# Performance work log

Hardware: AMD Instinct MI355X
Metric: run time of the kernel (lower is better)

The kernel has to match this reference:

```python
import jax, jax.numpy as jnp
import numpy as np

EPS = 1e-5
K = 3

def _bn(x, g, b):
    # training-mode BatchNorm2d: batch stats over (N,H,W), biased variance
    m = jnp.mean(x, axis=(0, 2, 3), keepdims=True)
    v = jnp.var(x, axis=(0, 2, 3), keepdims=True)
    return (x - m) * jax.lax.rsqrt(v + EPS) * g[None, :, None, None] + b[None, :, None, None]

def _gelu(x):
    return jax.nn.gelu(x, approximate=False)

def _dyn_dw(x, aw1, ab1, aw2, ab2):
    # dynamic depthwise conv: per-sample k^2 softmax weights shared over channels
    b, c, h, w = x.shape
    gap = jnp.mean(x, axis=(2, 3))                              # (b,c)
    h1 = jax.nn.relu(jnp.einsum('oc,bc->bo', aw1, gap) + ab1)   # (b,c//8)
    kw = jax.nn.softmax(jnp.einsum('oc,bc->bo', aw2, h1) + ab2, axis=1)  # (b,k^2)
    xp = jnp.pad(x, ((0, 0), (0, 0), (1, 1), (1, 1)))
    out = jnp.zeros_like(x)
    idx = 0
    for i in range(K):
        for j in range(K):
            out = out + kw[:, idx, None, None, None] * xp[:, :, i:i + h, j:j + w]
            idx += 1
    return out

def _channel_att(x, w1, w2):
    avg = jnp.mean(x, axis=(2, 3))        # (b,C)
    mx = jnp.max(x, axis=(2, 3))          # (b,C)
    def fc(v):
        return jnp.einsum('oc,bc->bo', w2, jax.nn.relu(jnp.einsum('oc,bc->bo', w1, v)))
    s = jax.nn.sigmoid(fc(avg) + fc(mx))  # (b,C)
    return s[:, :, None, None] * x

def _forward(x, w1, b1, g1, be1, aw1, ab1, aw2, ab2, g2, be2,
             ca_w1, ca_w2, pw, pb, g3, be3, sw, sb):
    b, n, d = x.shape
    h = w = int(np.sqrt(n))
    residual = x
    xi = jnp.transpose(x.reshape(b, h, w, d), (0, 3, 1, 2))       # (b,d,h,w)
    # pw_expand: 1x1 conv -> GELU -> BN
    y = jnp.einsum('oc,bchw->bohw', w1, xi) + b1[None, :, None, None]
    y = _bn(_gelu(y), g1, be1)                                    # (b,4d,h,w)
    # dw_conv: dynamic depthwise -> GELU -> BN -> channel attention
    y = _dyn_dw(y, aw1, ab1, aw2, ab2)
    y = _bn(_gelu(y), g2, be2)
    y = _channel_att(y, ca_w1, ca_w2)
    # spatial attention
    avg_o = jnp.mean(y, axis=1, keepdims=True)
    max_o = jnp.max(y, axis=1, keepdims=True)
    sp_in = jnp.concatenate([avg_o, max_o], axis=1)               # (b,2,h,w)
    sp = jax.lax.conv_general_dilated(sp_in, sw, (1, 1), ((3, 3), (3, 3)),
                                      dimension_numbers=('NCHW', 'OIHW', 'NCHW'))
    sp = jax.nn.sigmoid(sp + sb[None, :, None, None])
    y = y * sp
    # pw_project: 1x1 conv -> BN
    y = jnp.einsum('oc,bchw->bohw', pw, y) + pb[None, :, None, None]
    y = _bn(y, g3, be3)
    y = jnp.transpose(y, (0, 2, 3, 1)).reshape(b, n, d)
    return residual + y

def setup_inputs() -> dict:
    key = jax.random.key(0)
    ks = jax.random.split(key, 16)
    d, C = 256, 1024
    def rn(k, shape, fan):
        return jax.random.normal(k, shape, jnp.float32) * np.float32(np.sqrt(2.0 / fan))
    return {
        'x': jax.random.normal(ks[0], (8, 1024, d), jnp.float32),
        'w1': rn(ks[1], (C, d), d), 'b1': jnp.zeros((C,), jnp.float32),
        'g1': jnp.ones((C,), jnp.float32), 'be1': jnp.zeros((C,), jnp.float32),
        'aw1': rn(ks[2], (C // 8, C), C), 'ab1': jnp.zeros((C // 8,), jnp.float32),
        'aw2': rn(ks[3], (K * K, C // 8), C // 8), 'ab2': jnp.zeros((K * K,), jnp.float32),
        'g2': jnp.ones((C,), jnp.float32), 'be2': jnp.zeros((C,), jnp.float32),
        'ca_w1': rn(ks[4], (C // 16, C), C), 'ca_w2': rn(ks[5], (C, C // 16), C // 16),
        'pw': rn(ks[6], (d, C), C), 'pb': jnp.zeros((d,), jnp.float32),
        'g3': jnp.ones((d,), jnp.float32), 'be3': jnp.zeros((d,), jnp.float32),
        'sw': rn(ks[7], (1, 2, 7, 7), 2 * 49), 'sb': jnp.zeros((1,), jnp.float32),
    }

def reference(x, w1, b1, g1, be1, aw1, ab1, aw2, ab2, g2, be2,
              ca_w1, ca_w2, pw, pb, g3, be3, sw, sb):
    return _forward(x, w1, b1, g1, be1, aw1, ab1, aw2, ab2, g2, be2,
                    ca_w1, ca_w2, pw, pb, g3, be3, sw, sb)
```

## Files before the change

### kernel.cpp

```cpp
#include <hip/hip_runtime.h>
#include <math.h>

constexpr int B = 8;
constexpr int D = 256;
constexpr int C = 1024;
constexpr int H = 32, W = 32;
constexpr int P = H * W;
constexpr int M = B * P;
constexpr float EPS = 1e-5f;

typedef unsigned short u16;
typedef unsigned int u32;
typedef __attribute__((ext_vector_type(8))) short short8;
typedef __attribute__((ext_vector_type(4))) float floatx4;

constexpr size_t WS_CHSUM1 = 0;
constexpr size_t WS_CHSQ1  = 1024;
constexpr size_t WS_GAPSUM = 2048;
constexpr size_t WS_CHSUM3 = 10240;
constexpr size_t WS_CHSQ3  = 10496;
constexpr size_t WS_ACC_COUNT = 10752;
constexpr size_t WS_SCALE1 = 11264;
constexpr size_t WS_SHIFT1 = 12288;
constexpr size_t WS_KW     = 21504;
constexpr size_t WS_SCALE2 = 21760;
constexpr size_t WS_SHIFT2 = 22784;
constexpr size_t WS_AVGBN  = 23808;
constexpr size_t WS_MXBN   = 32000;
constexpr size_t WS_SATT   = 40192;
constexpr size_t WS_AVGO   = 48384;
constexpr size_t WS_MAXO   = 56576;
constexpr size_t WS_SP     = 64768;
constexpr size_t WS_PSUM2  = 73728;
constexpr size_t WS_PSQ2   = 335872;
constexpr size_t WS_PMAX2  = 598016;
constexpr size_t WS_PMIN2  = 860160;
constexpr size_t WS_PRE    = 1122304;
constexpr size_t WS_T1B    = 3219456;
constexpr size_t WS_T2B    = 7413760;
constexpr size_t WS_XB     = 11608064;
constexpr size_t WS_W1B    = 12656640;
constexpr size_t WS_PWB    = 12787712;
constexpr size_t WS_YB     = 12918784;

__device__ __forceinline__ float gelu_exact(float v) {
    return 0.5f * v * (1.0f + erff(v * 0.70710678118654752440f));
}

__device__ __forceinline__ u16 f2bf(float f) {
    u32 u = __float_as_uint(f);
    u += 0x7fff + ((u >> 16) & 1);
    return (u16)(u >> 16);
}

__device__ __forceinline__ float bf2f(u16 v) {
    return __uint_as_float(((u32)v) << 16);
}

__global__ __launch_bounds__(256) void cvt_all_kernel(const float* __restrict__ x,
                                                      const float* __restrict__ w1,
                                                      const float* __restrict__ pw,
                                                      u16* __restrict__ xb,
                                                      u16* __restrict__ w1b,
                                                      u16* __restrict__ pwb) {
    const int i = blockIdx.x * 256 + threadIdx.x;
    const float* src;
    u16* dst;
    int off;
    if (i < 524288)      { src = x;  dst = xb;  off = i; }
    else if (i < 589824) { src = w1; dst = w1b; off = i - 524288; }
    else                 { src = pw; dst = pwb; off = i - 589824; }
    const float4 v = *(const float4*)(src + (size_t)off * 4);
    uint2 o;
    o.x = ((u32)f2bf(v.x)) | ((u32)f2bf(v.y) << 16);
    o.y = ((u32)f2bf(v.z)) | ((u32)f2bf(v.w) << 16);
    *(uint2*)(dst + (size_t)off * 4) = o;
}

template<int KD, int EPI, int NS, int MB, int NB>
__global__ __launch_bounds__(256) void mfma_gemm_kernel(
    const u16* __restrict__ A,
    const u16* __restrict__ Bw,
    const float* __restrict__ bias,
    const float* __restrict__ rowscale,
    void* __restrict__ outv,
    float* __restrict__ csum,
    float* __restrict__ csq,
    float* __restrict__ gsum)
{
    constexpr int MI = MB / 32;
    constexpr int NJ = NB / 32;
    extern __shared__ u16 smem[];
    u16* As = smem;
    u16* Bs = smem + MB * 32;
    const int t = threadIdx.x;
    const int lane = t & 63;
    const int row0 = blockIdx.y * MB;
    const int col0 = blockIdx.x * NB;
    const int wv = t >> 6;
    const int wrow = (wv >> 1) * (MB / 2);
    const int wcol = (wv & 1) * (NB / 2);
    const int lm = lane & 15;
    const int lk8 = (lane >> 4) * 8;

    const int srow = t >> 2;
    const int scol = (t & 3) * 8;

    const u16* gA0 = A + (size_t)(row0 + srow) * KD + scol;
    const u16* gA1 = A + (size_t)(row0 + 64 + srow) * KD + scol;
    const u16* gB0 = Bw + (size_t)(col0 + srow) * KD + scol;

    const floatx4 zero = {0.f, 0.f, 0.f, 0.f};
    floatx4 acc[MI][NJ];
#pragma unroll
    for (int i = 0; i < MI; ++i)
#pragma unroll
        for (int j = 0; j < NJ; ++j) acc[i][j] = zero;

    for (int k0 = 0; k0 < KD; k0 += 32) {
        __builtin_amdgcn_global_load_lds(
            (const __attribute__((address_space(1))) void*)(gA0 + k0),
            (__attribute__((address_space(3))) void*)(As + t * 8), 16, 0, 0);
        if (MB == 128)
            __builtin_amdgcn_global_load_lds(
                (const __attribute__((address_space(1))) void*)(gA1 + k0),
                (__attribute__((address_space(3))) void*)(As + 2048 + t * 8), 16, 0, 0);
        __builtin_amdgcn_global_load_lds(
            (const __attribute__((address_space(1))) void*)(gB0 + k0),
            (__attribute__((address_space(3))) void*)(Bs + t * 8), 16, 0, 0);
        __syncthreads();
        short8 af[MI], bf[NJ];
#pragma unroll
        for (int i = 0; i < MI; ++i)
            af[i] = *(const short8*)(As + (wrow + i * 16 + lm) * 32 + lk8);
#pragma unroll
        for (int j = 0; j < NJ; ++j)
            bf[j] = *(const short8*)(Bs + (wcol + j * 16 + lm) * 32 + lk8);
#pragma unroll
        for (int i = 0; i < MI; ++i)
#pragma unroll
            for (int j = 0; j < NJ; ++j)
                acc[i][j] = __builtin_amdgcn_mfma_f32_16x16x32_bf16(af[i], bf[j], acc[i][j], 0, 0, 0);
        __syncthreads();
    }

    float colsum[NJ], colsq[NJ];
#pragma unroll
    for (int j = 0; j < NJ; ++j) { colsum[j] = 0.f; colsq[j] = 0.f; }

    if (EPI == 0) {
        u16* Cs = smem;
#pragma unroll
        for (int i = 0; i < MI; ++i) {
#pragma unroll
            for (int r = 0; r < 4; ++r) {
                const int lrow = wrow + i * 16 + (lane >> 4) * 4 + r;
#pragma unroll
                for (int j = 0; j < NJ; ++j) {
                    const int lcol = wcol + j * 16 + lm;
                    const float tv = gelu_exact(acc[i][j][r] + bias[col0 + lcol]);
                    Cs[lrow * NB + lcol] = f2bf(tv);
                    colsum[j] += tv;
                    colsq[j] = fmaf(tv, tv, colsq[j]);
                }
            }
        }
        __syncthreads();
        const int rr = t >> 1;
        const int hh = (t & 1) * 32;
        u16* outp = (u16*)outv + (size_t)(row0 + rr) * NS + col0 + hh;
#pragma unroll
        for (int k = 0; k < 4; ++k) {
            *(uint4*)(outp + k * 8) = *(const uint4*)(Cs + rr * NB + hh + k * 8);
        }
    } else {
#pragma unroll
        for (int i = 0; i < MI; ++i) {
#pragma unroll
            for (int r = 0; r < 4; ++r) {
                const int grow = row0 + wrow + i * 16 + (lane >> 4) * 4 + r;
                const float rs = rowscale[grow];
#pragma unroll
                for (int j = 0; j < NJ; ++j) {
                    const int gcol = col0 + wcol + j * 16 + lm;
                    const float tv = rs * acc[i][j][r] + bias[gcol];
                    ((float*)outv)[(size_t)grow * NS + gcol] = tv;
                    colsum[j] += tv;
                    colsq[j] = fmaf(tv, tv, colsq[j]);
                }
            }
        }
    }

    const int bb = (blockIdx.y * MB) >> 10;
#pragma unroll
    for (int j = 0; j < NJ; ++j) {
        float s = colsum[j];
        float q = colsq[j];
        s += __shfl_xor(s, 16); s += __shfl_xor(s, 32);
        q += __shfl_xor(q, 16); q += __shfl_xor(q, 32);
        if (lane < 16) {
            const int c = col0 + wcol + j * 16 + lm;
            atomicAdd(&csum[c], s);
            atomicAdd(&csq[c], q);
            if (EPI == 0) atomicAdd(&gsum[bb * NS + c], s);
        }
    }
}

__global__ __launch_bounds__(1024) void dynmlp_kernel(const float* __restrict__ chsum1,
                                                      const float* __restrict__ chsq1,
                                                      const float* __restrict__ gapsum,
                                                      const float* __restrict__ g1,
                                                      const float* __restrict__ be1,
                                                      const float* __restrict__ aw1,
                                                      const float* __restrict__ ab1,
                                                      const float* __restrict__ aw2,
                                                      const float* __restrict__ ab2,
                                                      float* __restrict__ scale1,
                                                      float* __restrict__ shift1,
                                                      float* __restrict__ kw) {
    const int b = blockIdx.x;
    const int t = threadIdx.x;
    const int wave = t >> 6, lane = t & 63;
    __shared__ float g[1024];
    __shared__ float h1[128];
    __shared__ float logits[12];
    {
        const float m = chsum1[t] * (1.0f / (float)M);
        const float var = chsq1[t] * (1.0f / (float)M) - m * m;
        const float rstd = rsqrtf(var + EPS);
        const float sc = rstd * g1[t];
        const float sh = be1[t] - m * sc;
        if (b == 0) { scale1[t] = sc; shift1[t] = sh; }
        g[t] = gapsum[b * C + t] * (1.0f / (float)P) * sc + sh;
    }
    __syncthreads();
#pragma unroll
    for (int k = 0; k < 8; ++k) {
        const int u = wave * 8 + k;
        const float4* wr = (const float4*)(aw1 + (size_t)u * C);
        float s = 0.f;
#pragma unroll
        for (int ch = 0; ch < 4; ++ch) {
            const float4 wv = wr[lane + 64 * ch];
            const float4 sv = *(const float4*)(g + 4 * lane + 256 * ch);
            s += wv.x * sv.x + wv.y * sv.y + wv.z * sv.z + wv.w * sv.w;
        }
#pragma unroll
        for (int off = 1; off < 64; off <<= 1) s += __shfl_xor(s, off);
        if (lane == 0) h1[u] = fmaxf(s + ab1[u], 0.f);
    }
    __syncthreads();
    if (wave < 9) {
        float s = aw2[wave * 128 + lane] * h1[lane]
                + aw2[wave * 128 + 64 + lane] * h1[64 + lane];
#pragma unroll
        for (int off = 1; off < 64; off <<= 1) s += __shfl_xor(s, off);
        if (lane == 0) logits[wave] = s + ab2[wave];
    }
    __syncthreads();
    if (t == 0) {
        float mx = logits[0];
        for (int i = 1; i < 9; ++i) mx = fmaxf(mx, logits[i]);
        float e[9], den = 0.f;
        for (int i = 0; i < 9; ++i) { e[i] = expf(logits[i] - mx); den += e[i]; }
        const float inv = 1.0f / den;
        for (int i = 0; i < 9; ++i) kw[b * 9 + i] = e[i] * inv;
    }
}

__global__ __launch_bounds__(256) void dwconv_kernel(const u16* __restrict__ t1b,
                                                     const float* __restrict__ scale1,
                                                     const float* __restrict__ shift1,
                                                     const float* __restrict__ kw,
                                                     u16* __restrict__ t2b,
                                                     float* __restrict__ psum,
                                                     float* __restrict__ psq,
                                                     float* __restrict__ pmax,
                                                     float* __restrict__ pmin) {
    const int b = blockIdx.y >> 5;
    const int h = blockIdx.y & 31;
    const int c0 = (blockIdx.x * 256 + threadIdx.x) * 2;
    float k[9];
#pragma unroll
    for (int i = 0; i < 9; ++i) k[i] = kw[b * 9 + i];
    const float sc0 = scale1[c0],     sh0 = shift1[c0];
    const float sc1 = scale1[c0 + 1], sh1 = shift1[c0 + 1];
    const u16* base = t1b + (size_t)b * P * C + c0;
    const bool rok[3] = { h > 0, true, h < H - 1 };

    float2 win[3][3];
    const float2 z = {0.f, 0.f};
#pragma unroll
    for (int ri = 0; ri < 3; ++ri) {
        win[ri][0] = z;
#pragma unroll
        for (int ci = 1; ci < 3; ++ci) {
            if (rok[ri]) {
                const u32 v = *(const u32*)(base + ((size_t)((h + ri - 1) * W + (ci - 1))) * C);
                float2 r;
                r.x = fmaf(bf2f((u16)(v & 0xffff)), sc0, sh0);
                r.y = fmaf(bf2f((u16)(v >> 16)),    sc1, sh1);
                win[ri][ci] = r;
            } else win[ri][ci] = z;
        }
    }

    float s0 = 0.f, q0 = 0.f, mx0 = -INFINITY, mn0 = INFINITY;
    float s1 = 0.f, q1 = 0.f, mx1 = -INFINITY, mn1 = INFINITY;
    for (int w = 0; w < W; ++w) {
        float a0 = 0.f, a1 = 0.f;
#pragma unroll
        for (int ri = 0; ri < 3; ++ri)
#pragma unroll
            for (int ci = 0; ci < 3; ++ci) {
                a0 = fmaf(k[ri * 3 + ci], win[ri][ci].x, a0);
                a1 = fmaf(k[ri * 3 + ci], win[ri][ci].y, a1);
            }
        const float y0 = gelu_exact(a0);
        const float y1 = gelu_exact(a1);
        *(u32*)(t2b + ((size_t)b * P + h * W + w) * C + c0) =
            ((u32)f2bf(y0)) | ((u32)f2bf(y1) << 16);
        s0 += y0; q0 = fmaf(y0, y0, q0); mx0 = fmaxf(mx0, y0); mn0 = fminf(mn0, y0);
        s1 += y1; q1 = fmaf(y1, y1, q1); mx1 = fmaxf(mx1, y1); mn1 = fminf(mn1, y1);
        if (w < W - 1) {
#pragma unroll
            for (int ri = 0; ri < 3; ++ri) {
                win[ri][0] = win[ri][1];
                win[ri][1] = win[ri][2];
                if (rok[ri] && (w + 2 < W)) {
                    const u32 v = *(const u32*)(base + ((size_t)((h + ri - 1) * W + (w + 2))) * C);
                    float2 r;
                    r.x = fmaf(bf2f((u16)(v & 0xffff)), sc0, sh0);
                    r.y = fmaf(bf2f((u16)(v >> 16)),    sc1, sh1);
                    win[ri][2] = r;
                } else win[ri][2] = z;
            }
        }
    }
    const int idx = b * 32 + h;
    psum[c0 * 256 + idx] = s0;  psum[(c0 + 1) * 256 + idx] = s1;
    psq [c0 * 256 + idx] = q0;  psq [(c0 + 1) * 256 + idx] = q1;
    pmax[c0 * 256 + idx] = mx0; pmax[(c0 + 1) * 256 + idx] = mx1;
    pmin[c0 * 256 + idx] = mn0; pmin[(c0 + 1) * 256 + idx] = mn1;
}

__global__ __launch_bounds__(256) void stats2_kernel(const float* __restrict__ psum,
                                                     const float* __restrict__ psq,
                                                     const float* __restrict__ pmax,
                                                     const float* __restrict__ pmin,
                                                     const float* __restrict__ g2,
                                                     const float* __restrict__ be2,
                                                     float* __restrict__ scale2,
                                                     float* __restrict__ shift2,
                                                     float* __restrict__ avgbn,
                                                     float* __restrict__ mxbn) {
    const int c = blockIdx.x;
    const int t = threadIdx.x;
    const int base = c * 256 + t;
    float s  = psum[base];
    float q  = psq[base];
    float mx = pmax[base];
    float mn = pmin[base];
#pragma unroll
    for (int off = 1; off < 32; off <<= 1) {
        s += __shfl_xor(s, off);
        q += __shfl_xor(q, off);
        mx = fmaxf(mx, __shfl_xor(mx, off));
        mn = fminf(mn, __shfl_xor(mn, off));
    }
    __shared__ float bs[8], bq[8], bmx[8], bmn[8];
    __shared__ float sc_sh[2];
    if ((t & 31) == 0) {
        const int b = t >> 5;
        bs[b] = s; bq[b] = q; bmx[b] = mx; bmn[b] = mn;
    }
    __syncthreads();
    if (t == 0) {
        float S = 0.f, Q = 0.f;
#pragma unroll
        for (int b = 0; b < 8; ++b) { S += bs[b]; Q += bq[b]; }
        const float m = S * (1.0f / (float)M);
        const float var = Q * (1.0f / (float)M) - m * m;
        const float rstd = rsqrtf(var + EPS);
        const float sc = rstd * g2[c];
        const float sh = be2[c] - m * sc;
        scale2[c] = sc;
        shift2[c] = sh;
        sc_sh[0] = sc; sc_sh[1] = sh;
    }
    __syncthreads();
    if (t < 8) {
        const float sc = sc_sh[0], sh = sc_sh[1];
        avgbn[t * C + c] = bs[t] * (1.0f / (float)P) * sc + sh;
        mxbn[t * C + c] = (sc >= 0.f ? bmx[t] : bmn[t]) * sc + sh;
    }
}

__global__ __launch_bounds__(1024) void chatt_kernel(const float* __restrict__ avgbn,
                                                     const float* __restrict__ mxbn,
                                                     const float* __restrict__ caw1,
                                                     const float* __restrict__ caw2,
                                                     float* __restrict__ s_att) {
    const int b = blockIdx.x;
    const int t = threadIdx.x;
    const int wave = t >> 6, lane = t & 63;
    __shared__ float la[1024], lx[1024], ha[64], hm[64];
    la[t] = avgbn[b * C + t];
    lx[t] = mxbn[b * C + t];
    __syncthreads();
#pragma unroll
    for (int k = 0; k < 8; ++k) {
        const int u = wave * 8 + k;
        const int row = u & 63;
        const float* src = (u < 64) ? la : lx;
        const float4* wr = (const float4*)(caw1 + (size_t)row * C);
        float s = 0.f;
#pragma unroll
        for (int ch = 0; ch < 4; ++ch) {
            const float4 wv = wr[lane + 64 * ch];
            const float4 sv = *(const float4*)(src + 4 * lane + 256 * ch);
            s += wv.x * sv.x + wv.y * sv.y + wv.z * sv.z + wv.w * sv.w;
        }
#pragma unroll
        for (int off = 1; off < 64; off <<= 1) s += __shfl_xor(s, off);
        if (lane == 0) {
            s = fmaxf(s, 0.f);
            if (u < 64) ha[row] = s; else hm[row] = s;
        }
    }
    __syncthreads();
    {
        const float4* w2 = (const float4*)(caw2 + (size_t)t * 64);
        float s = 0.f;
#pragma unroll
        for (int j = 0; j < 16; ++j) {
            const float4 wv = w2[j];
            s += wv.x * (ha[j * 4 + 0] + hm[j * 4 + 0]);
            s += wv.y * (ha[j * 4 + 1] + hm[j * 4 + 1]);
            s += wv.z * (ha[j * 4 + 2] + hm[j * 4 + 2]);
            s += wv.w * (ha[j * 4 + 3] + hm[j * 4 + 3]);
        }
        s_att[b * C + t] = 1.0f / (1.0f + expf(-s));
    }
}

__global__ __launch_bounds__(256) void yq_kernel(const u16* __restrict__ t2b,
                                                 const float* __restrict__ scale2,
                                                 const float* __restrict__ shift2,
                                                 const float* __restrict__ s_att,
                                                 u16* __restrict__ yb,
                                                 float* __restrict__ avg_o,
                                                 float* __restrict__ max_o) {
    const int row = blockIdx.x;
    const int b = row >> 10;
    const int t = threadIdx.x;
    const int c0 = t * 4;
    const uint2 vv = *(const uint2*)(t2b + (size_t)row * C + c0);
    const float v0 = bf2f((u16)(vv.x & 0xffff));
    const float v1 = bf2f((u16)(vv.x >> 16));
    const float v2 = bf2f((u16)(vv.y & 0xffff));
    const float v3 = bf2f((u16)(vv.y >> 16));
    const float4 sc = *(const float4*)(scale2 + c0);
    const float4 sh = *(const float4*)(shift2 + c0);
    const float4 sa = *(const float4*)(s_att + (size_t)b * C + c0);
    const float y0 = fmaf(v0, sc.x, sh.x) * sa.x;
    const float y1 = fmaf(v1, sc.y, sh.y) * sa.y;
    const float y2 = fmaf(v2, sc.z, sh.z) * sa.z;
    const float y3 = fmaf(v3, sc.w, sh.w) * sa.w;
    uint2 o;
    o.x = ((u32)f2bf(y0)) | ((u32)f2bf(y1) << 16);
    o.y = ((u32)f2bf(y2)) | ((u32)f2bf(y3) << 16);
    *(uint2*)(yb + (size_t)row * C + c0) = o;
    float s = (y0 + y1) + (y2 + y3);
    float mx = fmaxf(fmaxf(y0, y1), fmaxf(y2, y3));
#pragma unroll
    for (int off = 32; off > 0; off >>= 1) {
        s += __shfl_down(s, off);
        mx = fmaxf(mx, __shfl_down(mx, off));
    }
    __shared__ float ss[4], sm[4];
    const int wave = t >> 6, lane = t & 63;
    if (lane == 0) { ss[wave] = s; sm[wave] = mx; }
    __syncthreads();
    if (t == 0) {
        const float S = ss[0] + ss[1] + ss[2] + ss[3];
        const float Mx = fmaxf(fmaxf(sm[0], sm[1]), fmaxf(sm[2], sm[3]));
        avg_o[row] = S * (1.0f / (float)C);
        max_o[row] = Mx;
    }
}

__global__ __launch_bounds__(1024) void spconv_kernel(const float* __restrict__ avg_o,
                                                      const float* __restrict__ max_o,
                                                      const float* __restrict__ sw,
                                                      const float* __restrict__ sb,
                                                      float* __restrict__ sp) {
    const int b = blockIdx.x;
    const int t = threadIdx.x;
    __shared__ float pa[P], pm[P], wsh[98];
    pa[t] = avg_o[b * P + t];
    pm[t] = max_o[b * P + t];
    if (t < 98) wsh[t] = sw[t];
    const float sbv = sb[0];
    __syncthreads();
    const int h = t >> 5, w = t & 31;
    float acc = sbv;
#pragma unroll
    for (int i = 0; i < 7; ++i) {
        const int hh = h + i - 3;
        if (hh < 0 || hh >= H) continue;
#pragma unroll
        for (int j = 0; j < 7; ++j) {
            const int ww = w + j - 3;
            if (ww < 0 || ww >= W) continue;
            const int pidx = hh * W + ww;
            acc = fmaf(wsh[i * 7 + j], pa[pidx], acc);
            acc = fmaf(wsh[49 + i * 7 + j], pm[pidx], acc);
        }
    }
    sp[b * P + t] = 1.0f / (1.0f + expf(-acc));
}

__global__ __launch_bounds__(256) void final_kernel(const float* __restrict__ x,
                                                    const float* __restrict__ pre,
                                                    const float* __restrict__ chsum3,
                                                    const float* __restrict__ chsq3,
                                                    const float* __restrict__ g3,
                                                    const float* __restrict__ be3,
                                                    float* __restrict__ out) {
    __shared__ float lsc[256], lsh[256];
    const int t = threadIdx.x;
    {
        const float m = chsum3[t] * (1.0f / (float)M);
        const float var = chsq3[t] * (1.0f / (float)M) - m * m;
        const float rstd = rsqrtf(var + EPS);
        const float sc = rstd * g3[t];
        lsc[t] = sc;
        lsh[t] = be3[t] - m * sc;
    }
    __syncthreads();
    const int i = blockIdx.x * 256 + t;
    const int e = i * 4;
    const int d = e & 255;
    const float4 xv = *(const float4*)(x + e);
    const float4 pv = *(const float4*)(pre + e);
    const float4 sc = *(const float4*)(lsc + d);
    const float4 sh = *(const float4*)(lsh + d);
    float4 o;
    o.x = xv.x + fmaf(pv.x, sc.x, sh.x);
    o.y = xv.y + fmaf(pv.y, sc.y, sh.y);
    o.z = xv.z + fmaf(pv.z, sc.z, sh.z);
    o.w = xv.w + fmaf(pv.w, sc.w, sh.w);
    *(float4*)(out + e) = o;
}

extern "C" void kernel_launch(void* const* d_in, const int* in_sizes, int n_in,
                              void* d_out, int out_size, void* d_ws, size_t ws_size,
                              hipStream_t stream) {
    const float* x    = (const float*)d_in[0];
    const float* w1   = (const float*)d_in[1];
    const float* b1   = (const float*)d_in[2];
    const float* g1   = (const float*)d_in[3];
    const float* be1  = (const float*)d_in[4];
    const float* aw1  = (const float*)d_in[5];
    const float* ab1  = (const float*)d_in[6];
    const float* aw2  = (const float*)d_in[7];
    const float* ab2  = (const float*)d_in[8];
    const float* g2   = (const float*)d_in[9];
    const float* be2  = (const float*)d_in[10];
    const float* caw1 = (const float*)d_in[11];
    const float* caw2 = (const float*)d_in[12];
    const float* pw   = (const float*)d_in[13];
    const float* pb   = (const float*)d_in[14];
    const float* g3   = (const float*)d_in[15];
    const float* be3  = (const float*)d_in[16];
    const float* sw   = (const float*)d_in[17];
    const float* sb   = (const float*)d_in[18];
    float* out = (float*)d_out;
    float* ws = (float*)d_ws;

    hipMemsetAsync(ws, 0, WS_ACC_COUNT * sizeof(float), stream);

    float* chsum1  = ws + WS_CHSUM1;
    float* chsq1   = ws + WS_CHSQ1;
    float* gapsum  = ws + WS_GAPSUM;
    float* chsum3  = ws + WS_CHSUM3;
    float* chsq3   = ws + WS_CHSQ3;
    float* scale1  = ws + WS_SCALE1;
    float* shift1  = ws + WS_SHIFT1;
    float* kw      = ws + WS_KW;
    float* scale2  = ws + WS_SCALE2;
    float* shift2  = ws + WS_SHIFT2;
    float* avgbn   = ws + WS_AVGBN;
    float* mxbn    = ws + WS_MXBN;
    float* s_att   = ws + WS_SATT;
    float* avg_o   = ws + WS_AVGO;
    float* max_o   = ws + WS_MAXO;
    float* sp      = ws + WS_SP;
    float* psum2   = ws + WS_PSUM2;
    float* psq2    = ws + WS_PSQ2;
    float* pmax2   = ws + WS_PMAX2;
    float* pmin2   = ws + WS_PMIN2;
    float* pre     = ws + WS_PRE;
    u16* t1b = (u16*)(ws + WS_T1B);
    u16* t2b = (u16*)(ws + WS_T2B);
    u16* xb  = (u16*)(ws + WS_XB);
    u16* w1b = (u16*)(ws + WS_W1B);
    u16* pwb = (u16*)(ws + WS_PWB);
    u16* yb  = (u16*)(ws + WS_YB);

    cvt_all_kernel<<<dim3(2560), 256, 0, stream>>>(x, w1, pw, xb, w1b, pwb);
    mfma_gemm_kernel<256, 0, C, 128, 64><<<dim3(C / 64, M / 128), 256, 16384, stream>>>(
        xb, w1b, b1, nullptr, t1b, chsum1, chsq1, gapsum);
    dynmlp_kernel<<<dim3(B), 1024, 0, stream>>>(chsum1, chsq1, gapsum, g1, be1,
                                                aw1, ab1, aw2, ab2, scale1, shift1, kw);
    dwconv_kernel<<<dim3(C / 512, B * H), 256, 0, stream>>>(t1b, scale1, shift1, kw, t2b,
                                                            psum2, psq2, pmax2, pmin2);
    stats2_kernel<<<dim3(C), 256, 0, stream>>>(psum2, psq2, pmax2, pmin2, g2, be2,
                                               scale2, shift2, avgbn, mxbn);
    chatt_kernel<<<dim3(B), 1024, 0, stream>>>(avgbn, mxbn, caw1, caw2, s_att);
    yq_kernel<<<dim3(M), 256, 0, stream>>>(t2b, scale2, shift2, s_att, yb, avg_o, max_o);
    spconv_kernel<<<dim3(B), 1024, 0, stream>>>(avg_o, max_o, sw, sb, sp);
    mfma_gemm_kernel<1024, 1, D, 64, 64><<<dim3(D / 64, M / 64), 256, 8192, stream>>>(
        yb, pwb, pb, sp, pre, chsum3, chsq3, nullptr);
    final_kernel<<<dim3((M * D / 4) / 256), 256, 0, stream>>>(x, pre, chsum3, chsq3, g3, be3, out);
}
```

Measured before the change: 218.9 us.

## Replace dwconv partial-stat buffers with atomics and fold stats2 into chatt

The depthwise conv kernel now reduces its per-row sum, sum-of-squares, max and min straight into per-channel and per-batch accumulators with atomicAdd and atomicMax on order-preserving float keys, instead of writing partial arrays. The separate stats2 kernel is removed, and the channel-attention kernel now computes BN2 scale/shift and the pooled stats itself. The memset is folded into the convert kernel, which zeroes the accumulator region. This removes two launches and a large partial-stat round trip, at the cost of atomic contention and non-deterministic summation order.

```diff
diff --git a/kernel.cpp b/kernel.cpp
--- a/kernel.cpp
+++ b/kernel.cpp
@@ -19,29 +19,28 @@
 constexpr size_t WS_GAPSUM = 2048;
 constexpr size_t WS_CHSUM3 = 10240;
 constexpr size_t WS_CHSQ3  = 10496;
-constexpr size_t WS_ACC_COUNT = 10752;
-constexpr size_t WS_SCALE1 = 11264;
-constexpr size_t WS_SHIFT1 = 12288;
-constexpr size_t WS_KW     = 21504;
-constexpr size_t WS_SCALE2 = 21760;
-constexpr size_t WS_SHIFT2 = 22784;
-constexpr size_t WS_AVGBN  = 23808;
-constexpr size_t WS_MXBN   = 32000;
-constexpr size_t WS_SATT   = 40192;
-constexpr size_t WS_AVGO   = 48384;
-constexpr size_t WS_MAXO   = 56576;
-constexpr size_t WS_SP     = 64768;
-constexpr size_t WS_PSUM2  = 73728;
-constexpr size_t WS_PSQ2   = 335872;
-constexpr size_t WS_PMAX2  = 598016;
-constexpr size_t WS_PMIN2  = 860160;
-constexpr size_t WS_PRE    = 1122304;
-constexpr size_t WS_T1B    = 3219456;
-constexpr size_t WS_T2B    = 7413760;
-constexpr size_t WS_XB     = 11608064;
-constexpr size_t WS_W1B    = 12656640;
-constexpr size_t WS_PWB    = 12787712;
-constexpr size_t WS_YB     = 12918784;
+constexpr size_t WS_CHSUM2 = 10752;
+constexpr size_t WS_CHSQ2  = 11776;
+constexpr size_t WS_BSUM2  = 12800;
+constexpr size_t WS_UMAX2  = 20992;
+constexpr size_t WS_UMAXN2 = 29184;
+constexpr size_t WS_ACC_COUNT = 37376;
+constexpr size_t WS_SCALE1 = 37376;
+constexpr size_t WS_SHIFT1 = 38400;
+constexpr size_t WS_KW     = 39424;
+constexpr size_t WS_SCALE2 = 39680;
+constexpr size_t WS_SHIFT2 = 40704;
+constexpr size_t WS_SATT   = 41728;
+constexpr size_t WS_AVGO   = 49920;
+constexpr size_t WS_MAXO   = 58112;
+constexpr size_t WS_SP     = 66304;
+constexpr size_t WS_PRE    = 74496;
+constexpr size_t WS_T1B    = 2171648;
+constexpr size_t WS_T2B    = 6365952;
+constexpr size_t WS_XB     = 10560256;
+constexpr size_t WS_W1B    = 11608832;
+constexpr size_t WS_PWB    = 11739904;
+constexpr size_t WS_YB     = 11870976;
 
 __device__ __forceinline__ float gelu_exact(float v) {
     return 0.5f * v * (1.0f + erff(v * 0.70710678118654752440f));
@@ -55,6 +54,14 @@
 
 __device__ __forceinline__ float bf2f(u16 v) {
     return __uint_as_float(((u32)v) << 16);
+}
+
+__device__ __forceinline__ u32 fkey(float f) {
+    u32 u = __float_as_uint(f);
+    return (u & 0x80000000u) ? ~u : (u | 0x80000000u);
+}
+__device__ __forceinline__ float fkeyinv(u32 k) {
+    return __uint_as_float((k & 0x80000000u) ? (k ^ 0x80000000u) : ~k);
 }
 
 __global__ __launch_bounds__(256) void cvt_all_kernel(const float* __restrict__ x,
@@ -62,8 +69,10 @@
                                                       const float* __restrict__ pw,
                                                       u16* __restrict__ xb,
                                                       u16* __restrict__ w1b,
-                                                      u16* __restrict__ pwb) {
+                                                      u16* __restrict__ pwb,
+                                                      float* __restrict__ acc_zero) {
     const int i = blockIdx.x * 256 + threadIdx.x;
+    if (i < (int)WS_ACC_COUNT) acc_zero[i] = 0.f;
     const float* src;
     u16* dst;
     int off;
@@ -102,21 +111,17 @@
     const int wcol = (wv & 1) * (NB / 2);
     const int lm = lane & 15;
     const int lk8 = (lane >> 4) * 8;
-
     const int srow = t >> 2;
     const int scol = (t & 3) * 8;
-
     const u16* gA0 = A + (size_t)(row0 + srow) * KD + scol;
     const u16* gA1 = A + (size_t)(row0 + 64 + srow) * KD + scol;
     const u16* gB0 = Bw + (size_t)(col0 + srow) * KD + scol;
-
     const floatx4 zero = {0.f, 0.f, 0.f, 0.f};
     floatx4 acc[MI][NJ];
 #pragma unroll
     for (int i = 0; i < MI; ++i)
 #pragma unroll
         for (int j = 0; j < NJ; ++j) acc[i][j] = zero;
-
     for (int k0 = 0; k0 < KD; k0 += 32) {
         __builtin_amdgcn_global_load_lds(
             (const __attribute__((address_space(1))) void*)(gA0 + k0),
@@ -143,11 +148,9 @@
                 acc[i][j] = __builtin_amdgcn_mfma_f32_16x16x32_bf16(af[i], bf[j], acc[i][j], 0, 0, 0);
         __syncthreads();
     }
-
     float colsum[NJ], colsq[NJ];
 #pragma unroll
     for (int j = 0; j < NJ; ++j) { colsum[j] = 0.f; colsq[j] = 0.f; }
-
     if (EPI == 0) {
         u16* Cs = smem;
 #pragma unroll
@@ -191,7 +194,6 @@
             }
         }
     }
-
     const int bb = (blockIdx.y * MB) >> 10;
 #pragma unroll
     for (int j = 0; j < NJ; ++j) {
@@ -275,10 +277,11 @@
                                                      const float* __restrict__ shift1,
                                                      const float* __restrict__ kw,
                                                      u16* __restrict__ t2b,
-                                                     float* __restrict__ psum,
-                                                     float* __restrict__ psq,
-                                                     float* __restrict__ pmax,
-                                                     float* __restrict__ pmin) {
+                                                     float* __restrict__ chsum2,
+                                                     float* __restrict__ chsq2,
+                                                     float* __restrict__ bsum2,
+                                                     u32* __restrict__ umax2,
+                                                     u32* __restrict__ umaxn2) {
     const int b = blockIdx.y >> 5;
     const int h = blockIdx.y & 31;
     const int c0 = (blockIdx.x * 256 + threadIdx.x) * 2;
@@ -289,7 +292,6 @@
     const float sc1 = scale1[c0 + 1], sh1 = shift1[c0 + 1];
     const u16* base = t1b + (size_t)b * P * C + c0;
     const bool rok[3] = { h > 0, true, h < H - 1 };
-
     float2 win[3][3];
     const float2 z = {0.f, 0.f};
 #pragma unroll
@@ -306,7 +308,6 @@
             } else win[ri][ci] = z;
         }
     }
-
     float s0 = 0.f, q0 = 0.f, mx0 = -INFINITY, mn0 = INFINITY;
     float s1 = 0.f, q1 = 0.f, mx1 = -INFINITY, mn1 = INFINITY;
     for (int w = 0; w < W; ++w) {
@@ -339,76 +340,41 @@
             }
         }
     }
-    const int idx = b * 32 + h;
-    psum[c0 * 256 + idx] = s0;  psum[(c0 + 1) * 256 + idx] = s1;
-    psq [c0 * 256 + idx] = q0;  psq [(c0 + 1) * 256 + idx] = q1;
-    pmax[c0 * 256 + idx] = mx0; pmax[(c0 + 1) * 256 + idx] = mx1;
-    pmin[c0 * 256 + idx] = mn0; pmin[(c0 + 1) * 256 + idx] = mn1;
-}
-
-__global__ __launch_bounds__(256) void stats2_kernel(const float* __restrict__ psum,
-                                                     const float* __restrict__ psq,
-                                                     const float* __restrict__ pmax,
-                                                     const float* __restrict__ pmin,
+    atomicAdd(&chsum2[c0], s0);      atomicAdd(&chsum2[c0 + 1], s1);
+    atomicAdd(&chsq2[c0], q0);       atomicAdd(&chsq2[c0 + 1], q1);
+    atomicAdd(&bsum2[b * C + c0], s0);       atomicAdd(&bsum2[b * C + c0 + 1], s1);
+    atomicMax(&umax2[b * C + c0], fkey(mx0));   atomicMax(&umax2[b * C + c0 + 1], fkey(mx1));
+    atomicMax(&umaxn2[b * C + c0], fkey(-mn0)); atomicMax(&umaxn2[b * C + c0 + 1], fkey(-mn1));
+}
+
+__global__ __launch_bounds__(1024) void chatt_kernel(const float* __restrict__ chsum2,
+                                                     const float* __restrict__ chsq2,
+                                                     const float* __restrict__ bsum2,
+                                                     const u32* __restrict__ umax2,
+                                                     const u32* __restrict__ umaxn2,
                                                      const float* __restrict__ g2,
                                                      const float* __restrict__ be2,
+                                                     const float* __restrict__ caw1,
+                                                     const float* __restrict__ caw2,
                                                      float* __restrict__ scale2,
                                                      float* __restrict__ shift2,
-                                                     float* __restrict__ avgbn,
-                                                     float* __restrict__ mxbn) {
-    const int c = blockIdx.x;
-    const int t = threadIdx.x;
-    const int base = c * 256 + t;
-    float s  = psum[base];
-    float q  = psq[base];
-    float mx = pmax[base];
-    float mn = pmin[base];
-#pragma unroll
-    for (int off = 1; off < 32; off <<= 1) {
-        s += __shfl_xor(s, off);
-        q += __shfl_xor(q, off);
-        mx = fmaxf(mx, __shfl_xor(mx, off));
-        mn = fminf(mn, __shfl_xor(mn, off));
-    }
-    __shared__ float bs[8], bq[8], bmx[8], bmn[8];
-    __shared__ float sc_sh[2];
-    if ((t & 31) == 0) {
-        const int b = t >> 5;
-        bs[b] = s; bq[b] = q; bmx[b] = mx; bmn[b] = mn;
-    }
-    __syncthreads();
-    if (t == 0) {
-        float S = 0.f, Q = 0.f;
-#pragma unroll
-        for (int b = 0; b < 8; ++b) { S += bs[b]; Q += bq[b]; }
-        const float m = S * (1.0f / (float)M);
-        const float var = Q * (1.0f / (float)M) - m * m;
-        const float rstd = rsqrtf(var + EPS);
-        const float sc = rstd * g2[c];
-        const float sh = be2[c] - m * sc;
-        scale2[c] = sc;
-        shift2[c] = sh;
-        sc_sh[0] = sc; sc_sh[1] = sh;
-    }
-    __syncthreads();
-    if (t < 8) {
-        const float sc = sc_sh[0], sh = sc_sh[1];
-        avgbn[t * C + c] = bs[t] * (1.0f / (float)P) * sc + sh;
-        mxbn[t * C + c] = (sc >= 0.f ? bmx[t] : bmn[t]) * sc + sh;
-    }
-}
-
-__global__ __launch_bounds__(1024) void chatt_kernel(const float* __restrict__ avgbn,
-                                                     const float* __restrict__ mxbn,
-                                                     const float* __restrict__ caw1,
-                                                     const float* __restrict__ caw2,
                                                      float* __restrict__ s_att) {
     const int b = blockIdx.x;
     const int t = threadIdx.x;
     const int wave = t >> 6, lane = t & 63;
     __shared__ float la[1024], lx[1024], ha[64], hm[64];
-    la[t] = avgbn[b * C + t];
-    lx[t] = mxbn[b * C + t];
+    {
+        const float m = chsum2[t] * (1.0f / (float)M);
+        const float var = chsq2[t] * (1.0f / (float)M) - m * m;
+        const float rstd = rsqrtf(var + EPS);
+        const float sc = rstd * g2[t];
+        const float sh = be2[t] - m * sc;
+        if (b == 0) { scale2[t] = sc; shift2[t] = sh; }
+        la[t] = bsum2[b * C + t] * (1.0f / (float)P) * sc + sh;
+        const float mx = fkeyinv(umax2[b * C + t]);
+        const float mn = -fkeyinv(umaxn2[b * C + t]);
+        lx[t] = (sc >= 0.f ? mx : mn) * sc + sh;
+    }
     __syncthreads();
 #pragma unroll
     for (int k = 0; k < 8; ++k) {
@@ -581,28 +547,25 @@
     float* out = (float*)d_out;
     float* ws = (float*)d_ws;
 
-    hipMemsetAsync(ws, 0, WS_ACC_COUNT * sizeof(float), stream);
-
     float* chsum1  = ws + WS_CHSUM1;
     float* chsq1   = ws + WS_CHSQ1;
     float* gapsum  = ws + WS_GAPSUM;
     float* chsum3  = ws + WS_CHSUM3;
     float* chsq3   = ws + WS_CHSQ3;
+    float* chsum2  = ws + WS_CHSUM2;
+    float* chsq2   = ws + WS_CHSQ2;
+    float* bsum2   = ws + WS_BSUM2;
+    u32*   umax2   = (u32*)(ws + WS_UMAX2);
+    u32*   umaxn2  = (u32*)(ws + WS_UMAXN2);
     float* scale1  = ws + WS_SCALE1;
     float* shift1  = ws + WS_SHIFT1;
     float* kw      = ws + WS_KW;
     float* scale2  = ws + WS_SCALE2;
     float* shift2  = ws + WS_SHIFT2;
-    float* avgbn   = ws + WS_AVGBN;
-    float* mxbn    = ws + WS_MXBN;
     float* s_att   = ws + WS_SATT;
     float* avg_o   = ws + WS_AVGO;
     float* max_o   = ws + WS_MAXO;
     float* sp      = ws + WS_SP;
-    float* psum2   = ws + WS_PSUM2;
-    float* psq2    = ws + WS_PSQ2;
-    float* pmax2   = ws + WS_PMAX2;
-    float* pmin2   = ws + WS_PMIN2;
     float* pre     = ws + WS_PRE;
     u16* t1b = (u16*)(ws + WS_T1B);
     u16* t2b = (u16*)(ws + WS_T2B);
@@ -611,16 +574,15 @@
     u16* pwb = (u16*)(ws + WS_PWB);
     u16* yb  = (u16*)(ws + WS_YB);
 
-    cvt_all_kernel<<<dim3(2560), 256, 0, stream>>>(x, w1, pw, xb, w1b, pwb);
+    cvt_all_kernel<<<dim3(2560), 256, 0, stream>>>(x, w1, pw, xb, w1b, pwb, ws);
     mfma_gemm_kernel<256, 0, C, 128, 64><<<dim3(C / 64, M / 128), 256, 16384, stream>>>(
         xb, w1b, b1, nullptr, t1b, chsum1, chsq1, gapsum);
     dynmlp_kernel<<<dim3(B), 1024, 0, stream>>>(chsum1, chsq1, gapsum, g1, be1,
                                                 aw1, ab1, aw2, ab2, scale1, shift1, kw);
     dwconv_kernel<<<dim3(C / 512, B * H), 256, 0, stream>>>(t1b, scale1, shift1, kw, t2b,
-                                                            psum2, psq2, pmax2, pmin2);
-    stats2_kernel<<<dim3(C), 256, 0, stream>>>(psum2, psq2, pmax2, pmin2, g2, be2,
-                                               scale2, shift2, avgbn, mxbn);
-    chatt_kernel<<<dim3(B), 1024, 0, stream>>>(avgbn, mxbn, caw1, caw2, s_att);
+                                                            chsum2, chsq2, bsum2, umax2, umaxn2);
+    chatt_kernel<<<dim3(B), 1024, 0, stream>>>(chsum2, chsq2, bsum2, umax2, umaxn2,
+                                               g2, be2, caw1, caw2, scale2, shift2, s_att);
     yq_kernel<<<dim3(M), 256, 0, stream>>>(t2b, scale2, shift2, s_att, yb, avg_o, max_o);
     spconv_kernel<<<dim3(B), 1024, 0, stream>>>(avg_o, max_o, sw, sb, sp);
     mfma_gemm_kernel<1024, 1, D, 64, 64><<<dim3(D / 64, M / 64), 256, 8192, stream>>>(
```

Result: slower. 225.4 us (+3.0%).
